# Optimization experiments

Hardware: AMD Instinct MI355X
Metric: run time of the kernel (lower is better)

## Reference

```python
import jax, jax.numpy as jnp
import numpy as np

INV_SQRT2 = 0.7071067811865476  # Haar (db1) filter coefficient


def _haar_wavedec(x, level):
    """Haar (db1) multi-level DWT along axis=2 of x: [B,H,L,Dh].
    Returns [cA_n, cD_n, cD_{n-1}, ..., cD_1] (pywt.wavedec ordering).
    Exact match to pywt for L divisible by 2**level (no boundary padding needed)."""
    details = []
    a = x
    for _ in range(level):
        e, o = a[:, :, 0::2, :], a[:, :, 1::2, :]
        details.append((e - o) * INV_SQRT2)
        a = (e + o) * INV_SQRT2
    return [a] + details[::-1]


def _haar_idwt_step(a, d):
    """Single-level Haar inverse DWT along axis=2."""
    e = (a + d) * INV_SQRT2
    o = (a - d) * INV_SQRT2
    B, H, Lh, Dh = a.shape
    return jnp.stack([e, o], axis=3).reshape(B, H, 2 * Lh, Dh)


def setup_inputs() -> dict:
    key = jax.random.key(0)
    ks = jax.random.split(key, 6)
    B, L, D, H, M = 8, 4096, 1024, 16, 3
    Dh = D // H
    return {
        "query": jax.random.normal(ks[0], (B, L, D), jnp.float32),
        "W_qkv": jax.random.normal(ks[1], (3 * D, D), jnp.float32) * 0.02,
        "b_qkv": jnp.zeros((3 * D,), jnp.float32),
        "W_out": jax.random.normal(ks[2], (D, D), jnp.float32) * 0.02,
        "b_out": jnp.zeros((D,), jnp.float32),
        "weight_q": jax.random.normal(ks[3], (H, M, Dh), jnp.float32),
        "weight_v": jax.random.normal(ks[4], (H, M, Dh), jnp.float32),
    }


def reference(query, W_qkv, b_qkv, W_out, b_out, weight_q, weight_v):
    B, L, D = query.shape
    H, M, Dh = weight_q.shape  # n_heads, modes, head_dim

    qkv = query @ W_qkv.T + b_qkv               # [B,L,3D]; k chunk is unused (as in original)
    q = qkv[..., :D].reshape(B, L, H, Dh).transpose(0, 2, 1, 3)      # [B,H,L,Dh]
    v = qkv[..., 2 * D:].reshape(B, L, H, Dh).transpose(0, 2, 1, 3)  # [B,H,L,Dh]

    cq = _haar_wavedec(q, M)  # [cA_M, cD_M, ..., cD_1]
    cv = _haar_wavedec(v, M)

    # Weight the coarsest `modes` bands per head/channel, then multiply q*v in wavelet domain.
    prod = []
    for j in range(M):
        wq = weight_q[None, :, j, None, :]  # [1,H,1,Dh]
        wv = weight_v[None, :, j, None, :]
        prod.append((cq[j] * wq) * (cv[j] * wv))
    prod.append(cq[M] * cv[M])  # finest detail band, unweighted

    # Inverse DWT back to length L.
    a = prod[0]
    for d in prod[1:]:
        a = _haar_idwt_step(a, d)

    out = a.transpose(0, 2, 1, 3).reshape(B, L, D)
    return out @ W_out.T + b_out  # dropout is identity in eval
```

## Files before the change

### kernel.cpp

```cpp
#include <hip/hip_runtime.h>
#include <hip/hip_fp16.h>
#include <cstdint>
#include <cstddef>

typedef _Float16 f16;
typedef __attribute__((ext_vector_type(4))) _Float16 f16x4;
typedef __attribute__((ext_vector_type(8))) _Float16 f16x8;
typedef __attribute__((ext_vector_type(4))) float f32x4;

#define C_INV_SQRT2 0.70710678118654752440f

__device__ __forceinline__ void gld_lds16(const void* g, void* l) {
  __builtin_amdgcn_global_load_lds((const __attribute__((address_space(1))) void*)g,
                                   (__attribute__((address_space(3))) void*)l, 16, 0, 0);
}

__global__ __launch_bounds__(256) void cvt_f32_f16_k(const float* __restrict__ in,
                                                     f16* __restrict__ out, int n4) {
  int i = blockIdx.x * 256 + threadIdx.x;
  if (i >= n4) return;
  const float4 x = ((const float4*)in)[i];
  f16x4 y;
  y.x = (f16)x.x; y.y = (f16)x.y; y.z = (f16)x.z; y.w = (f16)x.w;
  ((f16x4*)out)[i] = y;
}

__global__ __launch_bounds__(256) void pack_wqv_k(const float* __restrict__ W,
                                                  const float* __restrict__ b,
                                                  f16* __restrict__ Wo,
                                                  float* __restrict__ bo) {
  int i = blockIdx.x * 256 + threadIdx.x;
  int n = i >> 8;
  int c = (i & 255) * 4;
  int sn = (n < 1024) ? n : (n + 1024);
  const float4 x = *(const float4*)(W + (size_t)sn * 1024 + c);
  f16x4 y; y.x = (f16)x.x; y.y = (f16)x.y; y.z = (f16)x.z; y.w = (f16)x.w;
  *(f16x4*)(Wo + (size_t)n * 1024 + c) = y;
  if (i < 2048) bo[i] = b[(i < 1024) ? i : (i + 1024)];
}


#define STAGE4(bufi, k0)                          \
  {                                               \
    f16* LA = &lds[bufi][0][0];                   \
    f16* LB = &lds[bufi][1][0];                   \
    gld_lds16(pGA0 + (k0), LA + dst0);            \
    gld_lds16(pGA1 + (k0), LA + dst1);            \
    gld_lds16(pGB0 + (k0), LB + dst0);            \
    gld_lds16(pGB1 + (k0), LB + dst1);            \
  }

template <typename CT>
__global__ __launch_bounds__(512, 2) void gemm256_k(const f16* __restrict__ A,
                                                    const f16* __restrict__ B,
                                                    const float* __restrict__ bias,
                                                    CT* __restrict__ C,
                                                    int M, int N, int K, int nbx) {
  __shared__ f16 lds[4][2][256 * 32];
  const int t = threadIdx.x;
  const int w = t >> 6, l = t & 63;
  const int wm = w >> 2, wn = w & 3;
  const int hi = l >> 4, lo = l & 15;

  const int nwg = gridDim.x;
  const int cpx = nwg >> 3;
  const int bid = blockIdx.x;
  const int nid = (bid & 7) * cpx + (bid >> 3);
  const int by = nid / nbx, bx = nid - by * nbx;
  const int m0 = by * 256, n0 = bx * 256;

  const f16* GA = A + (size_t)m0 * K;
  const f16* GB = B + (size_t)n0 * K;

  int rowS[2], chS[2];
#pragma unroll
  for (int i = 0; i < 2; i++) {
    const int u = i * 512 + t;
    rowS[i] = u >> 2;
    chS[i] = (u & 3) ^ ((u >> 3) & 3);
  }
  const f16* pGA0 = GA + (size_t)rowS[0] * K + chS[0] * 8;
  const f16* pGA1 = GA + (size_t)rowS[1] * K + chS[1] * 8;
  const f16* pGB0 = GB + (size_t)rowS[0] * K + chS[0] * 8;
  const f16* pGB1 = GB + (size_t)rowS[1] * K + chS[1] * 8;
  const int dst0 = (0 * 512 + w * 64) * 8;
  const int dst1 = (1 * 512 + w * 64) * 8;

  int offA[8], offB[4];
#pragma unroll
  for (int mi = 0; mi < 8; mi++) {
    const int r = wm * 128 + mi * 16 + lo;
    offA[mi] = r * 32 + ((hi ^ ((r >> 1) & 3)) << 3);
  }
#pragma unroll
  for (int nj = 0; nj < 4; nj++) {
    const int r = wn * 64 + nj * 16 + lo;
    offB[nj] = r * 32 + ((hi ^ ((r >> 1) & 3)) << 3);
  }

  f32x4 acc[8][4] = {};
  const int NS = K >> 5;

  STAGE4(0, 0);
  STAGE4(1, 32);
  STAGE4(2, 64);

  for (int s = 0; s < NS; ++s) {
    const int cur = s & 3;
    if (s < NS - 3) {
      STAGE4((s + 3) & 3, (s + 3) * 32);
      asm volatile("s_waitcnt vmcnt(12)" ::: "memory");
    } else if (s == NS - 3) {
      asm volatile("s_waitcnt vmcnt(8)" ::: "memory");
    } else if (s == NS - 2) {
      asm volatile("s_waitcnt vmcnt(4)" ::: "memory");
    } else {
      asm volatile("s_waitcnt vmcnt(0)" ::: "memory");
    }
    __builtin_amdgcn_s_barrier();
    __builtin_amdgcn_sched_barrier(0);
    const f16* pA = &lds[cur][0][0];
    const f16* pB = &lds[cur][1][0];
    f16x8 af[8], bf[4];
#pragma unroll
    for (int mi = 0; mi < 8; mi++) af[mi] = *(const f16x8*)(pA + offA[mi]);
#pragma unroll
    for (int nj = 0; nj < 4; nj++) bf[nj] = *(const f16x8*)(pB + offB[nj]);
    __builtin_amdgcn_s_setprio(1);
#pragma unroll
    for (int mi = 0; mi < 8; mi++)
#pragma unroll
      for (int nj = 0; nj < 4; nj++)
        acc[mi][nj] =
            __builtin_amdgcn_mfma_f32_16x16x32_f16(af[mi], bf[nj], acc[mi][nj], 0, 0, 0);
    __builtin_amdgcn_s_setprio(0);
    __builtin_amdgcn_sched_barrier(0);
    __builtin_amdgcn_s_barrier();
  }

#pragma unroll
  for (int mi = 0; mi < 8; mi++) {
#pragma unroll
    for (int nj = 0; nj < 4; nj++) {
      const int col = n0 + wn * 64 + nj * 16 + lo;
      const float bb = bias[col];
      const size_t base = (size_t)(m0 + wm * 128 + mi * 16 + hi * 4) * N + col;
#pragma unroll
      for (int r = 0; r < 4; r++) C[base + (size_t)r * N] = (CT)(acc[mi][nj][r] + bb);
    }
  }
}

__global__ __launch_bounds__(256) void dwt_middle_k(const f16* __restrict__ qv,
                                                    const float* __restrict__ wq,
                                                    const float* __restrict__ wv,
                                                    f16* __restrict__ out) {
  const int g = blockIdx.x;
  const int d0 = threadIdx.x * 4;
  const size_t m0 = (size_t)g * 8;

  f16x4 qr[8], vr[8], o[8];
#pragma unroll
  for (int i = 0; i < 8; i++) {
    qr[i] = *(const f16x4*)(qv + (m0 + i) * 2048 + d0);
    vr[i] = *(const f16x4*)(qv + (m0 + i) * 2048 + 1024 + d0);
  }
  const float c = C_INV_SQRT2;
#pragma unroll
  for (int dd = 0; dd < 4; dd++) {
    const int d = d0 + dd;
    const int h = d >> 6, dh = d & 63;
    float q[8], v[8];
#pragma unroll
    for (int i = 0; i < 8; i++) { q[i] = (float)qr[i][dd]; v[i] = (float)vr[i][dd]; }

    float qa1[4], qd1[4], va1[4], vd1[4];
#pragma unroll
    for (int i = 0; i < 4; i++) {
      qd1[i] = (q[2 * i] - q[2 * i + 1]) * c;
      qa1[i] = (q[2 * i] + q[2 * i + 1]) * c;
      vd1[i] = (v[2 * i] - v[2 * i + 1]) * c;
      va1[i] = (v[2 * i] + v[2 * i + 1]) * c;
    }
    float qa2[2], qd2[2], va2[2], vd2[2];
#pragma unroll
    for (int j = 0; j < 2; j++) {
      qd2[j] = (qa1[2 * j] - qa1[2 * j + 1]) * c;
      qa2[j] = (qa1[2 * j] + qa1[2 * j + 1]) * c;
      vd2[j] = (va1[2 * j] - va1[2 * j + 1]) * c;
      va2[j] = (va1[2 * j] + va1[2 * j + 1]) * c;
    }
    const float qd3 = (qa2[0] - qa2[1]) * c, qa3 = (qa2[0] + qa2[1]) * c;
    const float vd3 = (va2[0] - va2[1]) * c, va3 = (va2[0] + va2[1]) * c;

    const int wb = h * 192 + dh;
    const float wq0 = wq[wb], wq1 = wq[wb + 64], wq2 = wq[wb + 128];
    const float wv0 = wv[wb], wv1 = wv[wb + 64], wv2 = wv[wb + 128];

    const float pa = (qa3 * wq0) * (va3 * wv0);
    const float pd3 = (qd3 * wq1) * (vd3 * wv1);
    float pd2[2], pd1[4];
#pragma unroll
    for (int j = 0; j < 2; j++) pd2[j] = (qd2[j] * wq2) * (vd2[j] * wv2);
#pragma unroll
    for (int i = 0; i < 4; i++) pd1[i] = qd1[i] * vd1[i];

    float s2[2], s1[4];
    s2[0] = (pa + pd3) * c;
    s2[1] = (pa - pd3) * c;
#pragma unroll
    for (int j = 0; j < 2; j++) {
      s1[2 * j] = (s2[j] + pd2[j]) * c;
      s1[2 * j + 1] = (s2[j] - pd2[j]) * c;
    }
#pragma unroll
    for (int i = 0; i < 4; i++) {
      o[2 * i][dd] = (f16)((s1[i] + pd1[i]) * c);
      o[2 * i + 1][dd] = (f16)((s1[i] - pd1[i]) * c);
    }
  }
#pragma unroll
  for (int i = 0; i < 8; i++) *(f16x4*)(out + (m0 + i) * 1024 + d0) = o[i];
}

extern "C" void kernel_launch(void* const* d_in, const int* in_sizes, int n_in,
                              void* d_out, int out_size, void* d_ws, size_t ws_size,
                              hipStream_t stream) {
  (void)in_sizes; (void)n_in; (void)out_size; (void)ws_size;
  const float* query = (const float*)d_in[0];
  const float* W_qkv = (const float*)d_in[1];
  const float* b_qkv = (const float*)d_in[2];
  const float* W_out = (const float*)d_in[3];
  const float* b_out = (const float*)d_in[4];
  const float* wq = (const float*)d_in[5];
  const float* wv = (const float*)d_in[6];
  float* out = (float*)d_out;

  char* ws = (char*)d_ws;
  f16* qf16 = (f16*)ws;
  f16* Wqv = (f16*)(ws + 67108864);
  float* bqv = (float*)(ws + 67108864 + 4194304);
  f16* Wout = (f16*)(ws + 67108864 + 4194304 + 8192);
  f16* qv = (f16*)d_out;
  f16* a_f16 = qf16;

  cvt_f32_f16_k<<<dim3(8388608 / 256), dim3(256), 0, stream>>>(query, qf16, 8388608);
  pack_wqv_k<<<dim3(2048), dim3(256), 0, stream>>>(W_qkv, b_qkv, Wqv, bqv);
  cvt_f32_f16_k<<<dim3(262144 / 256), dim3(256), 0, stream>>>(W_out, Wout, 262144);
  gemm256_k<f16><<<dim3((2048 / 256) * (32768 / 256)), dim3(512), 0, stream>>>(
      qf16, Wqv, bqv, qv, 32768, 2048, 1024, 2048 / 256);
  dwt_middle_k<<<dim3(4096), dim3(256), 0, stream>>>(qv, wq, wv, a_f16);
  gemm256_k<float><<<dim3((1024 / 256) * (32768 / 256)), dim3(512), 0, stream>>>(
      a_f16, Wout, b_out, out, 32768, 1024, 1024, 1024 / 256);
}
```

Before: 305.5 us.

## Use 4-wave 128x128 warp tiles with register double-buffered LDS fragment prefetch

The GEMM kernel drops from 8 waves to 4 waves per 256x256 block, so each wave computes a 128x128 tile (8x8 MFMA accumulators). LDS fragments for the next k-step are read into a second register set while the current step's MFMAs run, and the barrier sequence is restructured so each step has a single barrier. The aim is a higher MFMA-to-LDS-read ratio and less barrier overhead. In exchange each wave needs far more registers (256 accumulator floats plus two fragment sets), and occupancy falls to one 4-wave block per CU, which raises the risk of spills and latency stalls.

```diff
diff --git a/kernel.cpp b/kernel.cpp
--- a/kernel.cpp
+++ b/kernel.cpp
@@ -40,18 +40,52 @@
 }
 
 
-#define STAGE4(bufi, k0)                          \
-  {                                               \
-    f16* LA = &lds[bufi][0][0];                   \
-    f16* LB = &lds[bufi][1][0];                   \
-    gld_lds16(pGA0 + (k0), LA + dst0);            \
-    gld_lds16(pGA1 + (k0), LA + dst1);            \
-    gld_lds16(pGB0 + (k0), LB + dst0);            \
-    gld_lds16(pGB1 + (k0), LB + dst1);            \
+#define STAGE4(bufi, k0)                                      \
+  {                                                           \
+    _Pragma("unroll") for (int i = 0; i < 4; i++)             \
+        gld_lds16(pGA[i] + (k0), &lds[bufi][0][0] + dstL[i]); \
+    _Pragma("unroll") for (int i = 0; i < 4; i++)             \
+        gld_lds16(pGB[i] + (k0), &lds[bufi][1][0] + dstL[i]); \
+  }
+
+#define READF(aF, bF, bufi)                                                  \
+  {                                                                          \
+    const f16* pA_ = &lds[bufi][0][0] + Abase;                               \
+    const f16* pB_ = &lds[bufi][1][0] + Bbase;                               \
+    _Pragma("unroll") for (int mi = 0; mi < 8; mi++)                         \
+        aF[mi] = *(const f16x8*)(pA_ + mi * 512);                            \
+    _Pragma("unroll") for (int nj = 0; nj < 8; nj++)                         \
+        bF[nj] = *(const f16x8*)(pB_ + nj * 512);                            \
+  }
+
+#define MFMA64(aF, bF)                                                       \
+  {                                                                          \
+    __builtin_amdgcn_s_setprio(1);                                           \
+    _Pragma("unroll") for (int mi = 0; mi < 8; mi++)                         \
+        _Pragma("unroll") for (int nj = 0; nj < 8; nj++)                     \
+            acc[mi][nj] = __builtin_amdgcn_mfma_f32_16x16x32_f16(            \
+                aF[mi], bF[nj], acc[mi][nj], 0, 0, 0);                       \
+    __builtin_amdgcn_s_setprio(0);                                           \
+  }
+
+#define ITER(s, aC, bC, aN, bN)                                      \
+  {                                                                  \
+    if ((s) < NS - 2) {                                              \
+      asm volatile("s_waitcnt vmcnt(8)" ::: "memory");               \
+    } else if ((s) == NS - 2) {                                      \
+      asm volatile("s_waitcnt vmcnt(0)" ::: "memory");               \
+    }                                                                \
+    __builtin_amdgcn_sched_barrier(0);                               \
+    __builtin_amdgcn_s_barrier();                                    \
+    __builtin_amdgcn_sched_barrier(0);                               \
+    if ((s) + 3 < NS) STAGE4(((s) + 3) & 3, ((s) + 3) * 32);         \
+    if ((s) + 1 < NS) READF(aN, bN, ((s) + 1) & 3);                  \
+    __builtin_amdgcn_sched_barrier(0);                               \
+    MFMA64(aC, bC);                                                  \
   }
 
 template <typename CT>
-__global__ __launch_bounds__(512, 2) void gemm256_k(const f16* __restrict__ A,
+__global__ __launch_bounds__(256, 1) void gemm256_k(const f16* __restrict__ A,
                                                     const f16* __restrict__ B,
                                                     const float* __restrict__ bias,
                                                     CT* __restrict__ C,
@@ -59,7 +93,7 @@
   __shared__ f16 lds[4][2][256 * 32];
   const int t = threadIdx.x;
   const int w = t >> 6, l = t & 63;
-  const int wm = w >> 2, wn = w & 3;
+  const int wm = w >> 1, wn = w & 1;
   const int hi = l >> 4, lo = l & 15;
 
   const int nwg = gridDim.x;
@@ -72,77 +106,45 @@
   const f16* GA = A + (size_t)m0 * K;
   const f16* GB = B + (size_t)n0 * K;
 
-  int rowS[2], chS[2];
-#pragma unroll
-  for (int i = 0; i < 2; i++) {
-    const int u = i * 512 + t;
-    rowS[i] = u >> 2;
-    chS[i] = (u & 3) ^ ((u >> 3) & 3);
-  }
-  const f16* pGA0 = GA + (size_t)rowS[0] * K + chS[0] * 8;
-  const f16* pGA1 = GA + (size_t)rowS[1] * K + chS[1] * 8;
-  const f16* pGB0 = GB + (size_t)rowS[0] * K + chS[0] * 8;
-  const f16* pGB1 = GB + (size_t)rowS[1] * K + chS[1] * 8;
-  const int dst0 = (0 * 512 + w * 64) * 8;
-  const int dst1 = (1 * 512 + w * 64) * 8;
-
-  int offA[8], offB[4];
-#pragma unroll
-  for (int mi = 0; mi < 8; mi++) {
-    const int r = wm * 128 + mi * 16 + lo;
-    offA[mi] = r * 32 + ((hi ^ ((r >> 1) & 3)) << 3);
-  }
-#pragma unroll
-  for (int nj = 0; nj < 4; nj++) {
-    const int r = wn * 64 + nj * 16 + lo;
-    offB[nj] = r * 32 + ((hi ^ ((r >> 1) & 3)) << 3);
-  }
-
-  f32x4 acc[8][4] = {};
+  const f16* pGA[4];
+  const f16* pGB[4];
+  int dstL[4];
+#pragma unroll
+  for (int i = 0; i < 4; i++) {
+    const int u = i * 256 + t;
+    const int row = u >> 2;
+    const int ch = (u & 3) ^ ((u >> 3) & 3);
+    pGA[i] = GA + (size_t)row * K + ch * 8;
+    pGB[i] = GB + (size_t)row * K + ch * 8;
+    dstL[i] = (i * 256 + w * 64) * 8;
+  }
+
+  const int swz = (hi ^ ((lo >> 1) & 3)) << 3;
+  const int Abase = (wm * 128 + lo) * 32 + swz;
+  const int Bbase = (wn * 128 + lo) * 32 + swz;
+
+  f32x4 acc[8][8] = {};
+  f16x8 aP[8], bP[8], aQ[8], bQ[8];
   const int NS = K >> 5;
 
   STAGE4(0, 0);
   STAGE4(1, 32);
   STAGE4(2, 64);
-
-  for (int s = 0; s < NS; ++s) {
-    const int cur = s & 3;
-    if (s < NS - 3) {
-      STAGE4((s + 3) & 3, (s + 3) * 32);
-      asm volatile("s_waitcnt vmcnt(12)" ::: "memory");
-    } else if (s == NS - 3) {
-      asm volatile("s_waitcnt vmcnt(8)" ::: "memory");
-    } else if (s == NS - 2) {
-      asm volatile("s_waitcnt vmcnt(4)" ::: "memory");
-    } else {
-      asm volatile("s_waitcnt vmcnt(0)" ::: "memory");
-    }
-    __builtin_amdgcn_s_barrier();
-    __builtin_amdgcn_sched_barrier(0);
-    const f16* pA = &lds[cur][0][0];
-    const f16* pB = &lds[cur][1][0];
-    f16x8 af[8], bf[4];
-#pragma unroll
-    for (int mi = 0; mi < 8; mi++) af[mi] = *(const f16x8*)(pA + offA[mi]);
-#pragma unroll
-    for (int nj = 0; nj < 4; nj++) bf[nj] = *(const f16x8*)(pB + offB[nj]);
-    __builtin_amdgcn_s_setprio(1);
-#pragma unroll
-    for (int mi = 0; mi < 8; mi++)
-#pragma unroll
-      for (int nj = 0; nj < 4; nj++)
-        acc[mi][nj] =
-            __builtin_amdgcn_mfma_f32_16x16x32_f16(af[mi], bf[nj], acc[mi][nj], 0, 0, 0);
-    __builtin_amdgcn_s_setprio(0);
-    __builtin_amdgcn_sched_barrier(0);
-    __builtin_amdgcn_s_barrier();
+  asm volatile("s_waitcnt vmcnt(16)" ::: "memory");
+  __builtin_amdgcn_s_barrier();
+  __builtin_amdgcn_sched_barrier(0);
+  READF(aP, bP, 0);
+
+  for (int s = 0; s < NS; s += 2) {
+    ITER(s, aP, bP, aQ, bQ);
+    ITER(s + 1, aQ, bQ, aP, bP);
   }
 
 #pragma unroll
   for (int mi = 0; mi < 8; mi++) {
 #pragma unroll
-    for (int nj = 0; nj < 4; nj++) {
-      const int col = n0 + wn * 64 + nj * 16 + lo;
+    for (int nj = 0; nj < 8; nj++) {
+      const int col = n0 + wn * 128 + nj * 16 + lo;
       const float bb = bias[col];
       const size_t base = (size_t)(m0 + wm * 128 + mi * 16 + hi * 4) * N + col;
 #pragma unroll
@@ -247,9 +249,9 @@
   cvt_f32_f16_k<<<dim3(8388608 / 256), dim3(256), 0, stream>>>(query, qf16, 8388608);
   pack_wqv_k<<<dim3(2048), dim3(256), 0, stream>>>(W_qkv, b_qkv, Wqv, bqv);
   cvt_f32_f16_k<<<dim3(262144 / 256), dim3(256), 0, stream>>>(W_out, Wout, 262144);
-  gemm256_k<f16><<<dim3((2048 / 256) * (32768 / 256)), dim3(512), 0, stream>>>(
+  gemm256_k<f16><<<dim3((2048 / 256) * (32768 / 256)), dim3(256), 0, stream>>>(
       qf16, Wqv, bqv, qv, 32768, 2048, 1024, 2048 / 256);
   dwt_middle_k<<<dim3(4096), dim3(256), 0, stream>>>(qv, wq, wv, a_f16);
-  gemm256_k<float><<<dim3((1024 / 256) * (32768 / 256)), dim3(512), 0, stream>>>(
+  gemm256_k<float><<<dim3((1024 / 256) * (32768 / 256)), dim3(256), 0, stream>>>(
       a_f16, Wout, b_out, out, 32768, 1024, 1024, 1024 / 256);
 }
```

Measured after the change: 520.9 us. 70.5% more time.

## Double-buffer A fragments in registers and use one barrier per GEMM k-step

Applied to the files above, without the earlier changes.

Restructures the fp16 GEMM main loop so the next k-step's A fragments are read from LDS into a second register set while MFMAs for the current step run. The loop is unrolled by two with ping-pong A buffers, and the global-to-LDS prefetch is issued after the barrier. This cuts the two barriers per k-step to one and relaxes the vmcnt waits. It aims to hide LDS read latency and barrier stalls, at the cost of more VGPR pressure. It also assumes an even number of k-steps.

```diff
diff --git a/kernel.cpp b/kernel.cpp
--- a/kernel.cpp
+++ b/kernel.cpp
@@ -50,6 +50,34 @@
     gld_lds16(pGB1 + (k0), LB + dst1);            \
   }
 
+#define ITER(s, aC, aN)                                                       \
+  {                                                                           \
+    if ((s) <= NS - 3) {                                                      \
+      asm volatile("s_waitcnt vmcnt(4)" ::: "memory");                        \
+    } else if ((s) == NS - 2) {                                               \
+      asm volatile("s_waitcnt vmcnt(0)" ::: "memory");                        \
+    }                                                                         \
+    __builtin_amdgcn_sched_barrier(0);                                        \
+    __builtin_amdgcn_s_barrier();                                             \
+    __builtin_amdgcn_sched_barrier(0);                                        \
+    const f16* pBc = &lds[(s) & 3][1][0];                                     \
+    f16x8 bF[4];                                                              \
+    _Pragma("unroll") for (int nj = 0; nj < 4; nj++)                          \
+        bF[nj] = *(const f16x8*)(pBc + offB[nj]);                             \
+    if ((s) + 1 < NS) {                                                       \
+      const f16* pAn = &lds[((s) + 1) & 3][0][0];                             \
+      _Pragma("unroll") for (int mi = 0; mi < 8; mi++)                        \
+          aN[mi] = *(const f16x8*)(pAn + offA[mi]);                           \
+    }                                                                         \
+    if ((s) + 3 < NS) STAGE4(((s) + 3) & 3, ((s) + 3) * 32);                  \
+    __builtin_amdgcn_s_setprio(1);                                            \
+    _Pragma("unroll") for (int mi = 0; mi < 8; mi++)                          \
+        _Pragma("unroll") for (int nj = 0; nj < 4; nj++)                      \
+            acc[mi][nj] = __builtin_amdgcn_mfma_f32_16x16x32_f16(             \
+                aC[mi], bF[nj], acc[mi][nj], 0, 0, 0);                        \
+    __builtin_amdgcn_s_setprio(0);                                            \
+  }
+
 template <typename CT>
 __global__ __launch_bounds__(512, 2) void gemm256_k(const f16* __restrict__ A,
                                                     const f16* __restrict__ B,
@@ -99,43 +127,24 @@
   }
 
   f32x4 acc[8][4] = {};
+  f16x8 aP[8], aQ[8];
   const int NS = K >> 5;
 
   STAGE4(0, 0);
   STAGE4(1, 32);
   STAGE4(2, 64);
-
-  for (int s = 0; s < NS; ++s) {
-    const int cur = s & 3;
-    if (s < NS - 3) {
-      STAGE4((s + 3) & 3, (s + 3) * 32);
-      asm volatile("s_waitcnt vmcnt(12)" ::: "memory");
-    } else if (s == NS - 3) {
-      asm volatile("s_waitcnt vmcnt(8)" ::: "memory");
-    } else if (s == NS - 2) {
-      asm volatile("s_waitcnt vmcnt(4)" ::: "memory");
-    } else {
-      asm volatile("s_waitcnt vmcnt(0)" ::: "memory");
-    }
-    __builtin_amdgcn_s_barrier();
-    __builtin_amdgcn_sched_barrier(0);
-    const f16* pA = &lds[cur][0][0];
-    const f16* pB = &lds[cur][1][0];
-    f16x8 af[8], bf[4];
-#pragma unroll
-    for (int mi = 0; mi < 8; mi++) af[mi] = *(const f16x8*)(pA + offA[mi]);
-#pragma unroll
-    for (int nj = 0; nj < 4; nj++) bf[nj] = *(const f16x8*)(pB + offB[nj]);
-    __builtin_amdgcn_s_setprio(1);
-#pragma unroll
-    for (int mi = 0; mi < 8; mi++)
-#pragma unroll
-      for (int nj = 0; nj < 4; nj++)
-        acc[mi][nj] =
-            __builtin_amdgcn_mfma_f32_16x16x32_f16(af[mi], bf[nj], acc[mi][nj], 0, 0, 0);
-    __builtin_amdgcn_s_setprio(0);
-    __builtin_amdgcn_sched_barrier(0);
-    __builtin_amdgcn_s_barrier();
+  asm volatile("s_waitcnt vmcnt(8)" ::: "memory");
+  __builtin_amdgcn_s_barrier();
+  __builtin_amdgcn_sched_barrier(0);
+  {
+    const f16* pA0 = &lds[0][0][0];
+#pragma unroll
+    for (int mi = 0; mi < 8; mi++) aP[mi] = *(const f16x8*)(pA0 + offA[mi]);
+  }
+
+  for (int s = 0; s < NS; s += 2) {
+    ITER(s, aP, aQ);
+    ITER(s + 1, aQ, aP);
   }
 
 #pragma unroll
```

Measured after the change: 296.2 us. -3.1%, faster.

## Restructure GEMM main loop into BK=64 double-buffer with interleaved half-tile staging

Applied to the files above, without the earlier changes.

Replaces the 4-stage BK=32 LDS ring with a 2-buffer BK=64 layout split into 128-row halves. Each iteration runs four MFMA phases, and global-to-LDS loads for the next tiles are issued between phases, with barriers placed so buffers can be refilled as soon as they are consumed. The LDS swizzle and fragment addressing change to 64-wide rows. The aim is to halve the barrier and wait count per K element and to overlap loads with MFMA more finely. In exchange there are more barriers per iteration, the prefetch depth is shallower, and more registers are needed to hold fragments.

```diff
diff --git a/kernel.cpp b/kernel.cpp
--- a/kernel.cpp
+++ b/kernel.cpp
@@ -40,15 +40,30 @@
 }
 
 
-#define STAGE4(bufi, k0)                          \
-  {                                               \
-    f16* LA = &lds[bufi][0][0];                   \
-    f16* LB = &lds[bufi][1][0];                   \
-    gld_lds16(pGA0 + (k0), LA + dst0);            \
-    gld_lds16(pGA1 + (k0), LA + dst1);            \
-    gld_lds16(pGB0 + (k0), LB + dst0);            \
-    gld_lds16(pGB1 + (k0), LB + dst1);            \
-  }
+#define STAGEH(bufi, mat, half, k0)                                              \
+  {                                                                              \
+    f16* Ld = &lds[bufi][mat][half][0];                                          \
+    const f16* Gp =                                                              \
+        ((mat) ? GB : GA) + (size_t)((half) * 128 + srow) * K + (k0) + sch * 8;  \
+    gld_lds16(Gp, Ld + (w * 64) * 8);                                            \
+    gld_lds16(Gp + (size_t)64 * K, Ld + (4096 + w * 64 * 8));                    \
+  }
+
+#define MFMA_PH(mi0)                                                             \
+  __builtin_amdgcn_s_setprio(1);                                                 \
+  _Pragma("unroll") for (int mm = (mi0); mm < (mi0) + 2; mm++)                   \
+      _Pragma("unroll") for (int nj = 0; nj < 4; nj++) {                         \
+    acc[mm][nj] = __builtin_amdgcn_mfma_f32_16x16x32_f16(aF[mm][0], bF[nj][0],   \
+                                                         acc[mm][nj], 0, 0, 0);  \
+    acc[mm][nj] = __builtin_amdgcn_mfma_f32_16x16x32_f16(aF[mm][1], bF[nj][1],   \
+                                                         acc[mm][nj], 0, 0, 0);  \
+  }                                                                              \
+  __builtin_amdgcn_s_setprio(0);
+
+#define BAR_SEQ()                       \
+  __builtin_amdgcn_sched_barrier(0);    \
+  __builtin_amdgcn_s_barrier();         \
+  __builtin_amdgcn_sched_barrier(0);
 
 template <typename CT>
 __global__ __launch_bounds__(512, 2) void gemm256_k(const f16* __restrict__ A,
@@ -56,7 +71,7 @@
                                                     const float* __restrict__ bias,
                                                     CT* __restrict__ C,
                                                     int M, int N, int K, int nbx) {
-  __shared__ f16 lds[4][2][256 * 32];
+  __shared__ f16 lds[2][2][2][128 * 64];
   const int t = threadIdx.x;
   const int w = t >> 6, l = t & 63;
   const int wm = w >> 2, wn = w & 3;
@@ -72,70 +87,69 @@
   const f16* GA = A + (size_t)m0 * K;
   const f16* GB = B + (size_t)n0 * K;
 
-  int rowS[2], chS[2];
-#pragma unroll
-  for (int i = 0; i < 2; i++) {
-    const int u = i * 512 + t;
-    rowS[i] = u >> 2;
-    chS[i] = (u & 3) ^ ((u >> 3) & 3);
-  }
-  const f16* pGA0 = GA + (size_t)rowS[0] * K + chS[0] * 8;
-  const f16* pGA1 = GA + (size_t)rowS[1] * K + chS[1] * 8;
-  const f16* pGB0 = GB + (size_t)rowS[0] * K + chS[0] * 8;
-  const f16* pGB1 = GB + (size_t)rowS[1] * K + chS[1] * 8;
-  const int dst0 = (0 * 512 + w * 64) * 8;
-  const int dst1 = (1 * 512 + w * 64) * 8;
-
-  int offA[8], offB[4];
-#pragma unroll
-  for (int mi = 0; mi < 8; mi++) {
-    const int r = wm * 128 + mi * 16 + lo;
-    offA[mi] = r * 32 + ((hi ^ ((r >> 1) & 3)) << 3);
-  }
-#pragma unroll
-  for (int nj = 0; nj < 4; nj++) {
-    const int r = wn * 64 + nj * 16 + lo;
-    offB[nj] = r * 32 + ((hi ^ ((r >> 1) & 3)) << 3);
-  }
+  const int srow = t >> 3;
+  const int sch = (t & 7) ^ (srow & 7);
+
+  const int colk0 = ((hi ^ (lo & 7)) << 3);
+  const int colk1 = (((4 | hi) ^ (lo & 7)) << 3);
 
   f32x4 acc[8][4] = {};
-  const int NS = K >> 5;
-
-  STAGE4(0, 0);
-  STAGE4(1, 32);
-  STAGE4(2, 64);
-
-  for (int s = 0; s < NS; ++s) {
-    const int cur = s & 3;
-    if (s < NS - 3) {
-      STAGE4((s + 3) & 3, (s + 3) * 32);
-      asm volatile("s_waitcnt vmcnt(12)" ::: "memory");
-    } else if (s == NS - 3) {
-      asm volatile("s_waitcnt vmcnt(8)" ::: "memory");
-    } else if (s == NS - 2) {
+  f16x8 aF[8][2], bF[4][2];
+  const int NT = K >> 6;
+
+  STAGEH(0, 0, 0, 0); STAGEH(0, 0, 1, 0);
+  STAGEH(0, 1, 0, 0); STAGEH(0, 1, 1, 0);
+  STAGEH(1, 0, 0, 64); STAGEH(1, 0, 1, 64);
+
+  for (int tt = 0; tt < NT; ++tt) {
+    const int buf = tt & 1;
+    const f16* pA = &lds[buf][0][wm][0] + lo * 64;
+    const f16* pB = &lds[buf][1][wn >> 1][0] + (wn & 1) * 4096 + lo * 64;
+    const f16* pA0 = pA + colk0;
+    const f16* pA1 = pA + colk1;
+    const f16* pB0 = pB + colk0;
+    const f16* pB1 = pB + colk1;
+
+    if (tt < NT - 1) {
       asm volatile("s_waitcnt vmcnt(4)" ::: "memory");
     } else {
       asm volatile("s_waitcnt vmcnt(0)" ::: "memory");
     }
-    __builtin_amdgcn_s_barrier();
-    __builtin_amdgcn_sched_barrier(0);
-    const f16* pA = &lds[cur][0][0];
-    const f16* pB = &lds[cur][1][0];
-    f16x8 af[8], bf[4];
-#pragma unroll
-    for (int mi = 0; mi < 8; mi++) af[mi] = *(const f16x8*)(pA + offA[mi]);
-#pragma unroll
-    for (int nj = 0; nj < 4; nj++) bf[nj] = *(const f16x8*)(pB + offB[nj]);
-    __builtin_amdgcn_s_setprio(1);
-#pragma unroll
-    for (int mi = 0; mi < 8; mi++)
-#pragma unroll
-      for (int nj = 0; nj < 4; nj++)
-        acc[mi][nj] =
-            __builtin_amdgcn_mfma_f32_16x16x32_f16(af[mi], bf[nj], acc[mi][nj], 0, 0, 0);
-    __builtin_amdgcn_s_setprio(0);
-    __builtin_amdgcn_sched_barrier(0);
-    __builtin_amdgcn_s_barrier();
+    BAR_SEQ();
+    aF[0][0] = *(const f16x8*)(pA0 + 0 * 1024);
+    aF[0][1] = *(const f16x8*)(pA1 + 0 * 1024);
+    aF[1][0] = *(const f16x8*)(pA0 + 1 * 1024);
+    aF[1][1] = *(const f16x8*)(pA1 + 1 * 1024);
+#pragma unroll
+    for (int nj = 0; nj < 4; nj++) {
+      bF[nj][0] = *(const f16x8*)(pB0 + nj * 1024);
+      bF[nj][1] = *(const f16x8*)(pB1 + nj * 1024);
+    }
+    aF[2][0] = *(const f16x8*)(pA0 + 2 * 1024);
+    aF[2][1] = *(const f16x8*)(pA1 + 2 * 1024);
+    aF[3][0] = *(const f16x8*)(pA0 + 3 * 1024);
+    aF[3][1] = *(const f16x8*)(pA1 + 3 * 1024);
+    if (tt + 1 < NT) STAGEH(buf ^ 1, 1, 0, (tt + 1) * 64);
+    MFMA_PH(0);
+
+    BAR_SEQ();
+#pragma unroll
+    for (int mi = 4; mi < 8; mi++) {
+      aF[mi][0] = *(const f16x8*)(pA0 + mi * 1024);
+      aF[mi][1] = *(const f16x8*)(pA1 + mi * 1024);
+    }
+    if (tt + 1 < NT) STAGEH(buf ^ 1, 1, 1, (tt + 1) * 64);
+    MFMA_PH(2);
+
+    asm volatile("s_waitcnt lgkmcnt(0)" ::: "memory");
+    BAR_SEQ();
+    if (tt + 2 < NT) STAGEH(buf, 0, 0, (tt + 2) * 64);
+    MFMA_PH(4);
+
+    asm volatile("s_waitcnt lgkmcnt(0)" ::: "memory");
+    BAR_SEQ();
+    if (tt + 2 < NT) STAGEH(buf, 0, 1, (tt + 2) * 64);
+    MFMA_PH(6);
   }
 
 #pragma unroll
```

Measured after the change: 286.1 us. 1.07x faster.
